# Kernel tuning notes

Hardware: AMD Instinct MI355X
Metric: run time of the kernel (lower is better)

## Reference

```python
import jax, jax.numpy as jnp
import numpy as np

B, S, D = 2, 2048, 1024
H, DH = 16, 64  # n_heads, d_head; D == H*DH
OUTPUT_SCALE = 1.0
EPS = 1e-08

def setup_inputs() -> dict:
    key = jax.random.key(0)
    k1, k2, k3 = jax.random.split(key, 3)
    x = jax.random.normal(k1, (B, S, D), dtype=jnp.float32)
    # causal-style mask would also work; use all-True [B,S,S] bool mask (True = attend)
    mask = jnp.tril(jnp.ones((S, S), dtype=bool))[None].repeat(B, axis=0)
    Wqkv = jax.random.normal(k2, (D, 3 * D), dtype=jnp.float32) * (1.0 / np.sqrt(D))
    Wo = jax.random.normal(k3, (D, D), dtype=jnp.float32) * (1.0 / np.sqrt(D))
    tau = jnp.full((H, 1, 1), float(DH) ** 0.5, dtype=jnp.float32)  # learned per-head temperature
    return {"x": x, "mask": mask, "Wqkv": Wqkv, "Wo": Wo, "tau": tau}

def reference(x, mask, Wqkv, Wo, tau):
    b, s, d = x.shape
    qkv = x @ Wqkv                                   # [B,S,3D]
    q, k, v = jnp.split(qkv, 3, axis=-1)
    # [B,S,D] -> [B,H,S,DH]
    q = q.reshape(b, s, H, DH).transpose(0, 2, 1, 3)
    k = k.reshape(b, s, H, DH).transpose(0, 2, 1, 3)
    v = v.reshape(b, s, H, DH).transpose(0, 2, 1, 3)
    # L2 normalize Q and K along head dim
    q = q / (jnp.linalg.norm(q, axis=-1, keepdims=True) + EPS)
    k = k / (jnp.linalg.norm(k, axis=-1, keepdims=True) + EPS)
    q = q * tau                                       # per-head learned temperature [H,1,1]
    logits = jnp.einsum('bhqd,bhkd->bhqk', q, k) / jnp.sqrt(jnp.float32(DH))
    m = mask if mask.ndim == 4 else mask[:, None, :, :]
    logits = jnp.where(m, logits, jnp.finfo(logits.dtype).min)
    w = jax.nn.softmax(logits, axis=-1)
    attn = jnp.einsum('bhqk,bhkd->bhqd', w, v)        # [B,H,S,DH]
    attn = attn.transpose(0, 2, 1, 3).reshape(b, s, d)
    return (attn @ Wo) * OUTPUT_SCALE
```

## Files before the change

### kernel.cpp

```cpp
#include <hip/hip_runtime.h>
#include <math.h>

#define BATCH 2
#define SEQ 2048
#define DMODEL 1024
#define NHEAD 16
#define DHEAD 64
#define QKV_COLS (3 * DMODEL)
#define EPS 1e-8f
#define LOG2E 1.44269504f

typedef short bf16x8 __attribute__((ext_vector_type(8)));
typedef float f32x4 __attribute__((ext_vector_type(4)));

static __device__ __forceinline__ unsigned short f2bf(float x) {
  unsigned u = __float_as_uint(x);
  u += 0x7fffu + ((u >> 16) & 1u);
  return (unsigned short)(u >> 16);
}

static __device__ __forceinline__ unsigned cvtpk(float lo, float hi) {
  unsigned r;
  asm("v_cvt_pk_bf16_f32 %0, %1, %2" : "=v"(r) : "v"(lo), "v"(hi));
  return r;
}

static __device__ __forceinline__ void async_ld16(const unsigned short* g,
                                                  unsigned short* l) {
  __builtin_amdgcn_global_load_lds(
      (const __attribute__((address_space(1))) void*)g,
      (__attribute__((address_space(3))) void*)(unsigned int)(unsigned long long)l,
      16, 0, 0);
}

__global__ __launch_bounds__(256) void prep_kernel(
    const float* __restrict__ x, unsigned short* __restrict__ xb,
    const float* __restrict__ W0, unsigned short* __restrict__ Wt0,
    const float* __restrict__ W1, unsigned short* __restrict__ Wt1) {
  __shared__ float tile[32][33];
  const int bid = blockIdx.x;
  if (bid < 4096) {
    const size_t i = ((size_t)bid * 256 + threadIdx.x) * 4;
    const float4 a = *(const float4*)(x + i);
    ushort4 r;
    r.x = f2bf(a.x); r.y = f2bf(a.y); r.z = f2bf(a.z); r.w = f2bf(a.w);
    *(ushort4*)(xb + i) = r;
    return;
  }
  const int bxx = bid - 4096;
  const int bxi = bxx & 127;
  const int k0 = (bxx >> 7) * 32;
  const float* W;
  unsigned short* Wt;
  int N, n0;
  if (bxi < 96) { W = W0; Wt = Wt0; N = QKV_COLS; n0 = bxi * 32; }
  else          { W = W1; Wt = Wt1; N = DMODEL;   n0 = (bxi - 96) * 32; }
  const int K = DMODEL;
  const int tx = threadIdx.x & 31, ty = threadIdx.x >> 5;
#pragma unroll
  for (int i = 0; i < 4; ++i)
    tile[ty + i * 8][tx] = W[(size_t)(k0 + ty + i * 8) * N + n0 + tx];
  __syncthreads();
#pragma unroll
  for (int i = 0; i < 4; ++i)
    Wt[(size_t)(n0 + ty + i * 8) * K + k0 + tx] = f2bf(tile[tx][ty + i * 8]);
}

__global__ __launch_bounds__(256) void sgemm_bf16_kernel(
    const unsigned short* __restrict__ A, const unsigned short* __restrict__ Bt,
    float* __restrict__ C, int M, int N, int K) {
  __shared__ unsigned short As[2][64 * 32];
  __shared__ unsigned short Bs[2][128 * 32];

  const int t = threadIdx.x;
  const int w = t >> 6;
  const int lane = t & 63;
  const int quad = lane >> 4;
  const int lr = lane & 15;
  const int rk = (lr >> 1) & 3;

  const int orig = blockIdx.y * gridDim.x + blockIdx.x;
  const int wg = (orig & 7) * 64 + (orig >> 3);
  const int bx = wg & 7, by = wg >> 3;
  const int m0 = by * 64;
  const int n0 = bx * 128;

  const int srow = lane >> 2;
  const int scol = ((lane & 3) ^ ((lane >> 3) & 3)) * 8;

  auto stage = [&](int k0, int bb) {
#pragma unroll
    for (int ii = 0; ii < 3; ++ii) {
      const int fi = w * 3 + ii;
      if (fi < 4) {
        async_ld16(A + (size_t)(m0 + fi * 16 + srow) * K + k0 + scol,
                   &As[bb][fi * 512]);
      } else {
        const int g = fi - 4;
        async_ld16(Bt + (size_t)(n0 + g * 16 + srow) * K + k0 + scol,
                   &Bs[bb][g * 512]);
      }
    }
  };

  f32x4 acc[4][2];
  const f32x4 zero4 = {0.f, 0.f, 0.f, 0.f};
#pragma unroll
  for (int i = 0; i < 4; ++i)
#pragma unroll
    for (int j = 0; j < 2; ++j) acc[i][j] = zero4;

  stage(0, 0);
  int bb = 0;
  for (int k0 = 0; k0 < K; k0 += 32, bb ^= 1) {
    __syncthreads();
    if (k0 + 32 < K) stage(k0 + 32, bb ^ 1);

    bf16x8 af[4], bfr[2];
#pragma unroll
    for (int i = 0; i < 4; ++i)
      af[i] = *(const bf16x8*)&As[bb][(i * 16 + lr) * 32 + ((quad ^ rk) * 8)];
#pragma unroll
    for (int j = 0; j < 2; ++j)
      bfr[j] = *(const bf16x8*)&Bs[bb][(w * 32 + j * 16 + lr) * 32 + ((quad ^ rk) * 8)];
#pragma unroll
    for (int i = 0; i < 4; ++i)
#pragma unroll
      for (int j = 0; j < 2; ++j)
        acc[i][j] = __builtin_amdgcn_mfma_f32_16x16x32_bf16(af[i], bfr[j], acc[i][j], 0, 0, 0);
  }

#pragma unroll
  for (int i = 0; i < 4; ++i)
#pragma unroll
    for (int r = 0; r < 4; ++r) {
      float* c = C + (size_t)(m0 + i * 16 + quad * 4 + r) * N + n0 + w * 32 + lr;
#pragma unroll
      for (int j = 0; j < 2; ++j) c[j * 16] = acc[i][j][r];
    }
}

__global__ __launch_bounds__(256) void qkv_gemm_norm_kernel(
    const unsigned short* __restrict__ A, const unsigned short* __restrict__ Bt,
    const float* __restrict__ tau,
    unsigned short* __restrict__ Qh, unsigned short* __restrict__ Kh,
    unsigned short* __restrict__ Vh) {
  __shared__ unsigned short As[2][128 * 32];
  __shared__ unsigned short Bs[2][128 * 32];

  const int K = DMODEL;
  const int t = threadIdx.x;
  const int w = t >> 6;
  const int lane = t & 63;
  const int quad = lane >> 4;
  const int lr = lane & 15;
  const int wr = w >> 1, wc = w & 1;
  const int rk = (lr >> 1) & 3;

  const int orig = blockIdx.y * gridDim.x + blockIdx.x;
  const int wg = (orig & 7) * 96 + (orig >> 3);
  const int bx = wg % 24, by = wg / 24;
  const int m0 = by * 128;
  const int n0 = bx * 128;

  const int srow = w * 32 + (lane >> 2);
  const int scol = ((lane & 3) ^ ((lane >> 3) & 3)) * 8;
  const unsigned short* ga = A + (size_t)(m0 + srow) * K + scol;
  const unsigned short* gb = Bt + (size_t)(n0 + srow) * K + scol;

  auto stage = [&](int k0, int bb) {
#pragma unroll
    for (int i = 0; i < 2; ++i) {
      async_ld16(ga + (size_t)(i * 16) * K + k0, &As[bb][(w * 32 + i * 16) * 32]);
      async_ld16(gb + (size_t)(i * 16) * K + k0, &Bs[bb][(w * 32 + i * 16) * 32]);
    }
  };

  f32x4 acc[4][4];
  const f32x4 zero4 = {0.f, 0.f, 0.f, 0.f};
#pragma unroll
  for (int i = 0; i < 4; ++i)
#pragma unroll
    for (int j = 0; j < 4; ++j) acc[i][j] = zero4;

  stage(0, 0);
  int bb = 0;
  for (int k0 = 0; k0 < K; k0 += 32, bb ^= 1) {
    __syncthreads();
    if (k0 + 32 < K) stage(k0 + 32, bb ^ 1);

    bf16x8 af[4], bfr[4];
#pragma unroll
    for (int i = 0; i < 4; ++i)
      af[i] = *(const bf16x8*)&As[bb][(wr * 64 + i * 16 + lr) * 32 + ((quad ^ rk) * 8)];
#pragma unroll
    for (int j = 0; j < 4; ++j)
      bfr[j] = *(const bf16x8*)&Bs[bb][(wc * 64 + j * 16 + lr) * 32 + ((quad ^ rk) * 8)];
#pragma unroll
    for (int i = 0; i < 4; ++i)
#pragma unroll
      for (int j = 0; j < 4; ++j)
        acc[i][j] = __builtin_amdgcn_mfma_f32_16x16x32_bf16(af[i], bfr[j], acc[i][j], 0, 0, 0);
  }

  const int col0 = n0 + wc * 64;
  const int which = col0 >> 10;
  const int h = (col0 & 1023) >> 6;
  const float tsc = tau[h] * 0.125f * LOG2E;
  unsigned short* dst = (which == 0) ? Qh : (which == 1) ? Kh : Vh;

#pragma unroll
  for (int i = 0; i < 4; ++i)
#pragma unroll
    for (int r = 0; r < 4; ++r) {
      const int s = m0 + wr * 64 + i * 16 + quad * 4 + r;
      unsigned short* ar =
          dst + (((size_t)((s >> 11) * NHEAD + h)) * SEQ + (s & 2047)) * DHEAD;
      float scale;
      if (which == 2) {
        scale = 1.0f;
      } else {
        float ss = 0.f;
#pragma unroll
        for (int j = 0; j < 4; ++j) ss += acc[i][j][r] * acc[i][j][r];
        ss += __shfl_xor(ss, 1, 16);
        ss += __shfl_xor(ss, 2, 16);
        ss += __shfl_xor(ss, 4, 16);
        ss += __shfl_xor(ss, 8, 16);
        scale = 1.0f / (sqrtf(ss) + EPS);
        if (which == 0) scale *= tsc;
      }
#pragma unroll
      for (int j = 0; j < 4; ++j) ar[j * 16 + lr] = f2bf(acc[i][j][r] * scale);
    }
}

__global__ __launch_bounds__(256) void vtrans_kernel(
    const unsigned short* __restrict__ Vh, unsigned short* __restrict__ Vt) {
  __shared__ unsigned short tile[64][72];
  const int bh = blockIdx.x;
  const int s0 = blockIdx.y * 64;
  const int t = threadIdx.x;
  const int sr = t >> 2;
  const int dc = (t & 3) * 16;
  const unsigned short* src = Vh + ((size_t)bh * SEQ + s0 + sr) * DHEAD + dc;
  *(bf16x8*)&tile[sr][dc]     = *(const bf16x8*)(src);
  *(bf16x8*)&tile[sr][dc + 8] = *(const bf16x8*)(src + 8);
  __syncthreads();
  const int dr = t >> 2;
  const int sc = (t & 3) * 16;
  unsigned short buf[16];
#pragma unroll
  for (int i = 0; i < 16; ++i) buf[i] = tile[sc + i][dr];
  unsigned short* dst = Vt + ((size_t)bh * DHEAD + dr) * SEQ + s0 + sc;
  *(bf16x8*)dst       = *(const bf16x8*)buf;
  *(bf16x8*)(dst + 8) = *(const bf16x8*)(buf + 8);
}

__global__ __launch_bounds__(256, 4) void attn_kernel(
    const unsigned short* __restrict__ Qh, const unsigned short* __restrict__ Kh,
    const unsigned short* __restrict__ Vt, unsigned short* __restrict__ attnb) {
  __shared__ unsigned short Ks[2][64 * 64];
  __shared__ unsigned short Vs[2][64 * 64];

  const int idx = blockIdx.x;
  const int bh = idx & 31;
  const int i2 = idx >> 5;
  const int seg = i2 >> 3, G = i2 & 7;
  const int qb = (seg == 0) ? 31 - G : (seg == 1) ? G : (seg == 2) ? 23 - G : 8 + G;
  const int b = bh >> 4;
  const int h = bh & 15;
  const int t = threadIdx.x;
  const int w = t >> 6;
  const int lane = t & 63;
  const int quad = lane >> 4;
  const int lr = lane & 15;
  const int sw = lr & 7;

  const unsigned short* Qp = Qh + (size_t)bh * SEQ * DHEAD;
  const unsigned short* Kp = Kh + (size_t)bh * SEQ * DHEAD;
  const unsigned short* Vp = Vt + (size_t)bh * DHEAD * SEQ;

  const int rrow = lane >> 3;
  const int swc = ((lane & 7) ^ rrow) * 8;
  const int f0 = w * 4;

  auto stage = [&](int k0, int bb) {
#pragma unroll
    for (int ii = 0; ii < 4; ++ii) {
      const int fi = f0 + ii;
      if (fi < 8) {
        async_ld16(Kp + (size_t)(k0 + fi * 8 + rrow) * DHEAD + swc,
                   &Ks[bb][fi * 512]);
      } else {
        const int g = fi - 8;
        async_ld16(Vp + (size_t)(g * 8 + rrow) * SEQ + k0 + swc,
                   &Vs[bb][g * 512]);
      }
    }
  };

  const f32x4 zero4 = {0.f, 0.f, 0.f, 0.f};
  f32x4 o[4];
  o[0] = o[1] = o[2] = o[3] = zero4;
  f32x4 ol = zero4;

  bf16x8 ones;
#pragma unroll
  for (int i = 0; i < 8; ++i) ones[i] = (short)0x3F80;

  const int q0 = qb * 64 + w * 16;
  const unsigned short* qr = Qp + (size_t)(q0 + lr) * DHEAD;
  const bf16x8 aq0 = *(const bf16x8*)(qr + quad * 8);
  const bf16x8 aq1 = *(const bf16x8*)(qr + 32 + quad * 8);
  const int qrow = q0 + lr;

  const int kend = qb * 64;

  stage(0, 0);
  int bb = 0;

  for (int k0 = 0; k0 <= kend; k0 += 64, bb ^= 1) {
    __syncthreads();
    if (k0 < kend) stage(k0 + 64, bb ^ 1);

    f32x4 c[4];
    __builtin_amdgcn_s_setprio(1);
#pragma unroll
    for (int kt = 0; kt < 4; ++kt) {
      const bf16x8 kf0 =
          *(const bf16x8*)&Ks[bb][(kt * 16 + lr) * 64 + ((quad ^ sw) * 8)];
      const bf16x8 kf1 =
          *(const bf16x8*)&Ks[bb][(kt * 16 + lr) * 64 + (((4 | quad) ^ sw) * 8)];
      f32x4 tt = __builtin_amdgcn_mfma_f32_16x16x32_bf16(kf0, aq0, zero4, 0, 0, 0);
      c[kt] = __builtin_amdgcn_mfma_f32_16x16x32_bf16(kf1, aq1, tt, 0, 0, 0);
    }
    __builtin_amdgcn_s_setprio(0);

    unsigned plo[4], phi[4];
    if (k0 == kend) {
#pragma unroll
      for (int kt = 0; kt < 4; ++kt) {
        float p[4];
#pragma unroll
        for (int r = 0; r < 4; ++r) {
          const int key = k0 + kt * 16 + quad * 4 + r;
          p[r] = (key <= qrow) ? exp2f(c[kt][r]) : 0.f;
        }
        plo[kt] = cvtpk(p[0], p[1]);
        phi[kt] = cvtpk(p[2], p[3]);
      }
    } else {
#pragma unroll
      for (int kt = 0; kt < 4; ++kt) {
        plo[kt] = cvtpk(exp2f(c[kt][0]), exp2f(c[kt][1]));
        phi[kt] = cvtpk(exp2f(c[kt][2]), exp2f(c[kt][3]));
      }
    }

#pragma unroll
    for (int c2 = 0; c2 < 2; ++c2) {
      unsigned aLo = plo[2 * c2],     aHi = phi[2 * c2];
      unsigned bLo = plo[2 * c2 + 1], bHi = phi[2 * c2 + 1];
      asm("v_permlane32_swap_b32 %0, %1" : "+v"(aLo), "+v"(bLo));
      asm("v_permlane32_swap_b32 %0, %1" : "+v"(aHi), "+v"(bHi));
      asm("v_permlane16_swap_b32 %0, %1" : "+v"(aLo), "+v"(bLo));
      asm("v_permlane16_swap_b32 %0, %1" : "+v"(aHi), "+v"(bHi));
      union { unsigned u[4]; bf16x8 v; } pk;
      pk.u[0] = aLo; pk.u[1] = aHi; pk.u[2] = bLo; pk.u[3] = bHi;
      const bf16x8 pa = pk.v;
      __builtin_amdgcn_s_setprio(1);
#pragma unroll
      for (int nt = 0; nt < 4; ++nt) {
        const bf16x8 vb = *(const bf16x8*)&Vs[bb][(nt * 16 + lr) * 64 +
                                                  (((c2 * 4 + quad) ^ sw) * 8)];
        o[nt] = __builtin_amdgcn_mfma_f32_16x16x32_bf16(pa, vb, o[nt], 0, 0, 0);
      }
      ol = __builtin_amdgcn_mfma_f32_16x16x32_bf16(pa, ones, ol, 0, 0, 0);
      __builtin_amdgcn_s_setprio(0);
    }
  }

#pragma unroll
  for (int r = 0; r < 4; ++r) {
    const float invr = 1.0f / ol[r];
    unsigned short* ar =
        attnb + ((size_t)(b * SEQ + q0 + quad * 4 + r)) * DMODEL + h * DHEAD;
#pragma unroll
    for (int nt = 0; nt < 4; ++nt) ar[nt * 16 + lr] = f2bf(o[nt][r] * invr);
  }
}

extern "C" void kernel_launch(void* const* d_in, const int* in_sizes, int n_in,
                              void* d_out, int out_size, void* d_ws, size_t ws_size,
                              hipStream_t stream) {
  const float* x    = (const float*)d_in[0];
  const float* Wqkv = (const float*)d_in[2];
  const float* Wo   = (const float*)d_in[3];
  const float* tau  = (const float*)d_in[4];
  float* out = (float*)d_out;

  unsigned short* attnb = (unsigned short*)d_ws;
  unsigned short* Qh = attnb + (size_t)BATCH * SEQ * DMODEL;
  unsigned short* Kh = Qh + (size_t)BATCH * NHEAD * SEQ * DHEAD;
  unsigned short* Vh = Kh + (size_t)BATCH * NHEAD * SEQ * DHEAD;
  unsigned short* Xb = Vh + (size_t)BATCH * NHEAD * SEQ * DHEAD;
  unsigned short* Wqkv_t = Xb + (size_t)BATCH * SEQ * DMODEL;
  unsigned short* Wo_t = Wqkv_t + (size_t)DMODEL * QKV_COLS;
  unsigned short* Vt = Wo_t + (size_t)DMODEL * DMODEL;

  const int M = BATCH * SEQ;

  prep_kernel<<<dim3(8192), 256, 0, stream>>>(x, Xb, Wqkv, Wqkv_t, Wo, Wo_t);

  qkv_gemm_norm_kernel<<<dim3(QKV_COLS / 128, M / 128), 256, 0, stream>>>(
      Xb, Wqkv_t, tau, Qh, Kh, Vh);

  vtrans_kernel<<<dim3(BATCH * NHEAD, SEQ / 64), 256, 0, stream>>>(Vh, Vt);

  attn_kernel<<<dim3(1024), 256, 0, stream>>>(Qh, Kh, Vt, attnb);

  sgemm_bf16_kernel<<<dim3(DMODEL / 128, M / 64), 256, 0, stream>>>(
      attnb, Wo_t, out, M, DMODEL, DMODEL);
}
```

Baseline: 193.0 us.

## Fuse V transpose into QKV GEMM epilogue and split-K output projection

The QKV GEMM epilogue now transposes V tiles through LDS and writes V directly in [bh, d, s] layout, which removes the separate vtrans kernel and one round trip of V through global memory. The output projection GEMM is split along K into two halves via blockIdx.z and accumulates with float atomicAdd into an output zeroed by a memset. This doubles the block count of that GEMM for better occupancy. It costs an extra memset, atomic traffic, and a nondeterministic summation order.

```diff
diff --git a/kernel.cpp b/kernel.cpp
--- a/kernel.cpp
+++ b/kernel.cpp
@@ -84,6 +84,8 @@
   const int bx = wg & 7, by = wg >> 3;
   const int m0 = by * 64;
   const int n0 = bx * 128;
+  const int KH = K >> 1;
+  const int ks0 = blockIdx.z * KH;
 
   const int srow = lane >> 2;
   const int scol = ((lane & 3) ^ ((lane >> 3) & 3)) * 8;
@@ -110,11 +112,11 @@
 #pragma unroll
     for (int j = 0; j < 2; ++j) acc[i][j] = zero4;
 
-  stage(0, 0);
+  stage(ks0, 0);
   int bb = 0;
-  for (int k0 = 0; k0 < K; k0 += 32, bb ^= 1) {
+  for (int k0 = ks0; k0 < ks0 + KH; k0 += 32, bb ^= 1) {
     __syncthreads();
-    if (k0 + 32 < K) stage(k0 + 32, bb ^ 1);
+    if (k0 + 32 < ks0 + KH) stage(k0 + 32, bb ^ 1);
 
     bf16x8 af[4], bfr[2];
 #pragma unroll
@@ -136,7 +138,7 @@
     for (int r = 0; r < 4; ++r) {
       float* c = C + (size_t)(m0 + i * 16 + quad * 4 + r) * N + n0 + w * 32 + lr;
 #pragma unroll
-      for (int j = 0; j < 2; ++j) c[j * 16] = acc[i][j][r];
+      for (int j = 0; j < 2; ++j) atomicAdd(&c[j * 16], acc[i][j][r]);
     }
 }
 
@@ -144,9 +146,10 @@
     const unsigned short* __restrict__ A, const unsigned short* __restrict__ Bt,
     const float* __restrict__ tau,
     unsigned short* __restrict__ Qh, unsigned short* __restrict__ Kh,
-    unsigned short* __restrict__ Vh) {
+    unsigned short* __restrict__ Vt) {
   __shared__ unsigned short As[2][128 * 32];
   __shared__ unsigned short Bs[2][128 * 32];
+  __shared__ unsigned short vtile[4][64 * 40];
 
   const int K = DMODEL;
   const int t = threadIdx.x;
@@ -206,20 +209,49 @@
   const int col0 = n0 + wc * 64;
   const int which = col0 >> 10;
   const int h = (col0 & 1023) >> 6;
-  const float tsc = tau[h] * 0.125f * LOG2E;
-  unsigned short* dst = (which == 0) ? Qh : (which == 1) ? Kh : Vh;
-
-#pragma unroll
-  for (int i = 0; i < 4; ++i)
-#pragma unroll
-    for (int r = 0; r < 4; ++r) {
-      const int s = m0 + wr * 64 + i * 16 + quad * 4 + r;
-      unsigned short* ar =
-          dst + (((size_t)((s >> 11) * NHEAD + h)) * SEQ + (s & 2047)) * DHEAD;
-      float scale;
-      if (which == 2) {
-        scale = 1.0f;
-      } else {
+
+  if (which == 2) {
+    const int sglob0 = m0 + wr * 64;
+    const int b2 = sglob0 >> 11;
+    const int sin0 = sglob0 & 2047;
+    const int bh2 = b2 * NHEAD + h;
+    unsigned short* vt = &vtile[w][0];
+#pragma unroll
+    for (int hh = 0; hh < 2; ++hh) {
+#pragma unroll
+      for (int i2 = 0; i2 < 2; ++i2) {
+        const int i = hh * 2 + i2;
+#pragma unroll
+        for (int j = 0; j < 4; ++j) {
+          ushort4 v4;
+          v4.x = f2bf(acc[i][j][0]); v4.y = f2bf(acc[i][j][1]);
+          v4.z = f2bf(acc[i][j][2]); v4.w = f2bf(acc[i][j][3]);
+          *(ushort4*)&vt[(j * 16 + lr) * 40 + i2 * 16 + quad * 4] = v4;
+        }
+      }
+      asm volatile("s_waitcnt lgkmcnt(0)" ::: "memory");
+      __builtin_amdgcn_sched_barrier(0);
+      const int dr = lane;
+      unsigned short* dst =
+          Vt + ((size_t)bh2 * DHEAD + dr) * SEQ + sin0 + hh * 32;
+#pragma unroll
+      for (int qs = 0; qs < 4; ++qs)
+        *(bf16x8*)(dst + qs * 8) = *(const bf16x8*)&vt[dr * 40 + qs * 8];
+      if (hh == 0) {
+        asm volatile("s_waitcnt lgkmcnt(0)" ::: "memory");
+        __builtin_amdgcn_sched_barrier(0);
+      }
+    }
+  } else {
+    const float tsc = tau[h] * 0.125f * LOG2E;
+    unsigned short* dst = (which == 0) ? Qh : Kh;
+#pragma unroll
+    for (int i = 0; i < 4; ++i)
+#pragma unroll
+      for (int r = 0; r < 4; ++r) {
+        const int s = m0 + wr * 64 + i * 16 + quad * 4 + r;
+        unsigned short* ar =
+            dst + (((size_t)((s >> 11) * NHEAD + h)) * SEQ + (s & 2047)) * DHEAD;
         float ss = 0.f;
 #pragma unroll
         for (int j = 0; j < 4; ++j) ss += acc[i][j][r] * acc[i][j][r];
@@ -227,34 +259,12 @@
         ss += __shfl_xor(ss, 2, 16);
         ss += __shfl_xor(ss, 4, 16);
         ss += __shfl_xor(ss, 8, 16);
-        scale = 1.0f / (sqrtf(ss) + EPS);
+        float scale = 1.0f / (sqrtf(ss) + EPS);
         if (which == 0) scale *= tsc;
-      }
-#pragma unroll
-      for (int j = 0; j < 4; ++j) ar[j * 16 + lr] = f2bf(acc[i][j][r] * scale);
-    }
-}
-
-__global__ __launch_bounds__(256) void vtrans_kernel(
-    const unsigned short* __restrict__ Vh, unsigned short* __restrict__ Vt) {
-  __shared__ unsigned short tile[64][72];
-  const int bh = blockIdx.x;
-  const int s0 = blockIdx.y * 64;
-  const int t = threadIdx.x;
-  const int sr = t >> 2;
-  const int dc = (t & 3) * 16;
-  const unsigned short* src = Vh + ((size_t)bh * SEQ + s0 + sr) * DHEAD + dc;
-  *(bf16x8*)&tile[sr][dc]     = *(const bf16x8*)(src);
-  *(bf16x8*)&tile[sr][dc + 8] = *(const bf16x8*)(src + 8);
-  __syncthreads();
-  const int dr = t >> 2;
-  const int sc = (t & 3) * 16;
-  unsigned short buf[16];
-#pragma unroll
-  for (int i = 0; i < 16; ++i) buf[i] = tile[sc + i][dr];
-  unsigned short* dst = Vt + ((size_t)bh * DHEAD + dr) * SEQ + s0 + sc;
-  *(bf16x8*)dst       = *(const bf16x8*)buf;
-  *(bf16x8*)(dst + 8) = *(const bf16x8*)(buf + 8);
+#pragma unroll
+        for (int j = 0; j < 4; ++j) ar[j * 16 + lr] = f2bf(acc[i][j][r] * scale);
+      }
+  }
 }
 
 __global__ __launch_bounds__(256, 4) void attn_kernel(
@@ -414,12 +424,11 @@
   prep_kernel<<<dim3(8192), 256, 0, stream>>>(x, Xb, Wqkv, Wqkv_t, Wo, Wo_t);
 
   qkv_gemm_norm_kernel<<<dim3(QKV_COLS / 128, M / 128), 256, 0, stream>>>(
-      Xb, Wqkv_t, tau, Qh, Kh, Vh);
-
-  vtrans_kernel<<<dim3(BATCH * NHEAD, SEQ / 64), 256, 0, stream>>>(Vh, Vt);
+      Xb, Wqkv_t, tau, Qh, Kh, Vt);
 
   attn_kernel<<<dim3(1024), 256, 0, stream>>>(Qh, Kh, Vt, attnb);
 
-  sgemm_bf16_kernel<<<dim3(DMODEL / 128, M / 64), 256, 0, stream>>>(
+  hipMemsetAsync(out, 0, (size_t)M * DMODEL * sizeof(float), stream);
+  sgemm_bf16_kernel<<<dim3(8, 64, 2), 256, 0, stream>>>(
       attnb, Wo_t, out, M, DMODEL, DMODEL);
 }
```

New measurement: 210.2 us. 1.09x slower.

## Process two query tiles per attention block to reuse K/V loads

Applied to the files above, without the earlier changes.

Each attention block now handles 128 query rows as two 64-row sub-tiles, A and B. The K and V fragments staged in shared memory and read into registers are shared by both sub-tiles. This halves global and LDS traffic per query row and halves the grid to 512 blocks, with a simpler heavy-first ordering of query blocks. The cost is doubled accumulator registers, a launch-bounds occupancy hint lowered from 4 to 2, and fewer blocks to balance across compute units.

```diff
diff --git a/kernel.cpp b/kernel.cpp
--- a/kernel.cpp
+++ b/kernel.cpp
@@ -257,7 +257,7 @@
   *(bf16x8*)(dst + 8) = *(const bf16x8*)(buf + 8);
 }
 
-__global__ __launch_bounds__(256, 4) void attn_kernel(
+__global__ __launch_bounds__(256, 2) void attn_kernel(
     const unsigned short* __restrict__ Qh, const unsigned short* __restrict__ Kh,
     const unsigned short* __restrict__ Vt, unsigned short* __restrict__ attnb) {
   __shared__ unsigned short Ks[2][64 * 64];
@@ -265,9 +265,8 @@
 
   const int idx = blockIdx.x;
   const int bh = idx & 31;
-  const int i2 = idx >> 5;
-  const int seg = i2 >> 3, G = i2 & 7;
-  const int qb = (seg == 0) ? 31 - G : (seg == 1) ? G : (seg == 2) ? 23 - G : 8 + G;
+  const int sl = idx >> 5;
+  const int qb = (sl < 8) ? 15 - sl : sl - 8;
   const int b = bh >> 4;
   const int h = bh & 15;
   const int t = threadIdx.x;
@@ -301,44 +300,33 @@
   };
 
   const f32x4 zero4 = {0.f, 0.f, 0.f, 0.f};
-  f32x4 o[4];
-  o[0] = o[1] = o[2] = o[3] = zero4;
-  f32x4 ol = zero4;
+  f32x4 oA[4], oB[4];
+  oA[0] = oA[1] = oA[2] = oA[3] = zero4;
+  oB[0] = oB[1] = oB[2] = oB[3] = zero4;
+  f32x4 olA = zero4, olB = zero4;
 
   bf16x8 ones;
 #pragma unroll
   for (int i = 0; i < 8; ++i) ones[i] = (short)0x3F80;
 
-  const int q0 = qb * 64 + w * 16;
-  const unsigned short* qr = Qp + (size_t)(q0 + lr) * DHEAD;
-  const bf16x8 aq0 = *(const bf16x8*)(qr + quad * 8);
-  const bf16x8 aq1 = *(const bf16x8*)(qr + 32 + quad * 8);
-  const int qrow = q0 + lr;
-
-  const int kend = qb * 64;
-
-  stage(0, 0);
-  int bb = 0;
-
-  for (int k0 = 0; k0 <= kend; k0 += 64, bb ^= 1) {
-    __syncthreads();
-    if (k0 < kend) stage(k0 + 64, bb ^ 1);
-
-    f32x4 c[4];
-    __builtin_amdgcn_s_setprio(1);
-#pragma unroll
-    for (int kt = 0; kt < 4; ++kt) {
-      const bf16x8 kf0 =
-          *(const bf16x8*)&Ks[bb][(kt * 16 + lr) * 64 + ((quad ^ sw) * 8)];
-      const bf16x8 kf1 =
-          *(const bf16x8*)&Ks[bb][(kt * 16 + lr) * 64 + (((4 | quad) ^ sw) * 8)];
-      f32x4 tt = __builtin_amdgcn_mfma_f32_16x16x32_bf16(kf0, aq0, zero4, 0, 0, 0);
-      c[kt] = __builtin_amdgcn_mfma_f32_16x16x32_bf16(kf1, aq1, tt, 0, 0, 0);
-    }
-    __builtin_amdgcn_s_setprio(0);
-
-    unsigned plo[4], phi[4];
-    if (k0 == kend) {
+  const int qbase = qb * 128;
+  const int q0A = qbase + w * 16;
+  const int q0B = qbase + 64 + w * 16;
+  const unsigned short* qrA = Qp + (size_t)(q0A + lr) * DHEAD;
+  const unsigned short* qrB = Qp + (size_t)(q0B + lr) * DHEAD;
+  const bf16x8 aqA0 = *(const bf16x8*)(qrA + quad * 8);
+  const bf16x8 aqA1 = *(const bf16x8*)(qrA + 32 + quad * 8);
+  const bf16x8 aqB0 = *(const bf16x8*)(qrB + quad * 8);
+  const bf16x8 aqB1 = *(const bf16x8*)(qrB + 32 + quad * 8);
+  const int qrowA = q0A + lr;
+  const int qrowB = q0B + lr;
+
+  const int kA = qbase;
+  const int kend = qbase + 64;
+
+  auto smpack = [&](const f32x4* c, int k0, bool msk, int qrow,
+                    unsigned* plo, unsigned* phi) {
+    if (msk) {
 #pragma unroll
       for (int kt = 0; kt < 4; ++kt) {
         float p[4];
@@ -357,38 +345,91 @@
         phi[kt] = cvtpk(exp2f(c[kt][2]), exp2f(c[kt][3]));
       }
     }
+  };
+
+  auto pvacc = [&](const unsigned* plo, const unsigned* phi, int c2,
+                   const bf16x8* vb, f32x4* o, f32x4& ol) {
+    unsigned aLo = plo[2 * c2],     aHi = phi[2 * c2];
+    unsigned bLo = plo[2 * c2 + 1], bHi = phi[2 * c2 + 1];
+    asm("v_permlane32_swap_b32 %0, %1" : "+v"(aLo), "+v"(bLo));
+    asm("v_permlane32_swap_b32 %0, %1" : "+v"(aHi), "+v"(bHi));
+    asm("v_permlane16_swap_b32 %0, %1" : "+v"(aLo), "+v"(bLo));
+    asm("v_permlane16_swap_b32 %0, %1" : "+v"(aHi), "+v"(bHi));
+    union { unsigned u[4]; bf16x8 v; } pk;
+    pk.u[0] = aLo; pk.u[1] = aHi; pk.u[2] = bLo; pk.u[3] = bHi;
+    const bf16x8 pa = pk.v;
+    __builtin_amdgcn_s_setprio(1);
+#pragma unroll
+    for (int nt = 0; nt < 4; ++nt)
+      o[nt] = __builtin_amdgcn_mfma_f32_16x16x32_bf16(pa, vb[nt], o[nt], 0, 0, 0);
+    ol = __builtin_amdgcn_mfma_f32_16x16x32_bf16(pa, ones, ol, 0, 0, 0);
+    __builtin_amdgcn_s_setprio(0);
+  };
+
+  stage(0, 0);
+  int bb = 0;
+
+  for (int k0 = 0; k0 <= kend; k0 += 64, bb ^= 1) {
+    __syncthreads();
+    if (k0 < kend) stage(k0 + 64, bb ^ 1);
+
+    bf16x8 kf0[4], kf1[4];
+#pragma unroll
+    for (int kt = 0; kt < 4; ++kt) {
+      kf0[kt] = *(const bf16x8*)&Ks[bb][(kt * 16 + lr) * 64 + ((quad ^ sw) * 8)];
+      kf1[kt] = *(const bf16x8*)&Ks[bb][(kt * 16 + lr) * 64 + (((4 | quad) ^ sw) * 8)];
+    }
+
+    const bool actA = (k0 <= kA);
+    unsigned ploA[4], phiA[4], ploB[4], phiB[4];
+
+    if (actA) {
+      f32x4 c[4];
+      __builtin_amdgcn_s_setprio(1);
+#pragma unroll
+      for (int kt = 0; kt < 4; ++kt) {
+        f32x4 tt = __builtin_amdgcn_mfma_f32_16x16x32_bf16(kf0[kt], aqA0, zero4, 0, 0, 0);
+        c[kt] = __builtin_amdgcn_mfma_f32_16x16x32_bf16(kf1[kt], aqA1, tt, 0, 0, 0);
+      }
+      __builtin_amdgcn_s_setprio(0);
+      smpack(c, k0, k0 == kA, qrowA, ploA, phiA);
+    }
+    {
+      f32x4 c[4];
+      __builtin_amdgcn_s_setprio(1);
+#pragma unroll
+      for (int kt = 0; kt < 4; ++kt) {
+        f32x4 tt = __builtin_amdgcn_mfma_f32_16x16x32_bf16(kf0[kt], aqB0, zero4, 0, 0, 0);
+        c[kt] = __builtin_amdgcn_mfma_f32_16x16x32_bf16(kf1[kt], aqB1, tt, 0, 0, 0);
+      }
+      __builtin_amdgcn_s_setprio(0);
+      smpack(c, k0, k0 == kend, qrowB, ploB, phiB);
+    }
 
 #pragma unroll
     for (int c2 = 0; c2 < 2; ++c2) {
-      unsigned aLo = plo[2 * c2],     aHi = phi[2 * c2];
-      unsigned bLo = plo[2 * c2 + 1], bHi = phi[2 * c2 + 1];
-      asm("v_permlane32_swap_b32 %0, %1" : "+v"(aLo), "+v"(bLo));
-      asm("v_permlane32_swap_b32 %0, %1" : "+v"(aHi), "+v"(bHi));
-      asm("v_permlane16_swap_b32 %0, %1" : "+v"(aLo), "+v"(bLo));
-      asm("v_permlane16_swap_b32 %0, %1" : "+v"(aHi), "+v"(bHi));
-      union { unsigned u[4]; bf16x8 v; } pk;
-      pk.u[0] = aLo; pk.u[1] = aHi; pk.u[2] = bLo; pk.u[3] = bHi;
-      const bf16x8 pa = pk.v;
-      __builtin_amdgcn_s_setprio(1);
-#pragma unroll
-      for (int nt = 0; nt < 4; ++nt) {
-        const bf16x8 vb = *(const bf16x8*)&Vs[bb][(nt * 16 + lr) * 64 +
-                                                  (((c2 * 4 + quad) ^ sw) * 8)];
-        o[nt] = __builtin_amdgcn_mfma_f32_16x16x32_bf16(pa, vb, o[nt], 0, 0, 0);
-      }
-      ol = __builtin_amdgcn_mfma_f32_16x16x32_bf16(pa, ones, ol, 0, 0, 0);
-      __builtin_amdgcn_s_setprio(0);
+      bf16x8 vb[4];
+#pragma unroll
+      for (int nt = 0; nt < 4; ++nt)
+        vb[nt] = *(const bf16x8*)&Vs[bb][(nt * 16 + lr) * 64 +
+                                         (((c2 * 4 + quad) ^ sw) * 8)];
+      if (actA) pvacc(ploA, phiA, c2, vb, oA, olA);
+      pvacc(ploB, phiB, c2, vb, oB, olB);
     }
   }
 
-#pragma unroll
-  for (int r = 0; r < 4; ++r) {
-    const float invr = 1.0f / ol[r];
-    unsigned short* ar =
-        attnb + ((size_t)(b * SEQ + q0 + quad * 4 + r)) * DMODEL + h * DHEAD;
-#pragma unroll
-    for (int nt = 0; nt < 4; ++nt) ar[nt * 16 + lr] = f2bf(o[nt][r] * invr);
-  }
+  auto epi = [&](int q0g, const f32x4* o, const f32x4& ol) {
+#pragma unroll
+    for (int r = 0; r < 4; ++r) {
+      const float invr = 1.0f / ol[r];
+      unsigned short* ar =
+          attnb + ((size_t)(b * SEQ + q0g + quad * 4 + r)) * DMODEL + h * DHEAD;
+#pragma unroll
+      for (int nt = 0; nt < 4; ++nt) ar[nt * 16 + lr] = f2bf(o[nt][r] * invr);
+    }
+  };
+  epi(q0A, oA, olA);
+  epi(q0B, oB, olB);
 }
 
 extern "C" void kernel_launch(void* const* d_in, const int* in_sizes, int n_in,
@@ -418,7 +459,7 @@
 
   vtrans_kernel<<<dim3(BATCH * NHEAD, SEQ / 64), 256, 0, stream>>>(Vh, Vt);
 
-  attn_kernel<<<dim3(1024), 256, 0, stream>>>(Qh, Kh, Vt, attnb);
+  attn_kernel<<<dim3(512), 256, 0, stream>>>(Qh, Kh, Vt, attnb);
 
   sgemm_bf16_kernel<<<dim3(DMODEL / 128, M / 64), 256, 0, stream>>>(
       attnb, Wo_t, out, M, DMODEL, DMODEL);
```

Measured after the change: 202.1 us. 1.05x slower.
